# Kernel tuning notes

Measured on AMD Instinct MI355X. Metric: run time of the kernel, lower is better.

## Reference

```python
import jax, jax.numpy as jnp
import numpy as np

B, S, HID = 2, 2048, 2048
NH, NKV = 32, 8
HD = HID // NH          # 64
G = NH // NKV           # 4 query heads per kv head
ROPE_BASE = 10000.0


def _rope_cos_sin(seq_len, head_dim, dtype):
    inv_freq = 1.0 / (ROPE_BASE ** (jnp.arange(0, head_dim, 2, dtype=jnp.float32) / head_dim))
    freqs = jnp.arange(seq_len, dtype=jnp.float32)[:, None] * inv_freq[None, :]  # [S, HD/2]
    cos = jnp.cos(freqs)
    sin = jnp.sin(freqs)
    # torch code does cos.repeat(1, 2): tile along last dim -> [S, HD]
    cos = jnp.concatenate([cos, cos], axis=-1).astype(dtype)
    sin = jnp.concatenate([sin, sin], axis=-1).astype(dtype)
    return cos, sin


def _rotate_half(x):
    x1, x2 = jnp.split(x, 2, axis=-1)
    return jnp.concatenate([-x2, x1], axis=-1)


def setup_inputs() -> dict:
    key = jax.random.key(0)
    ks = jax.random.split(key, 5)
    sc = 0.02
    return {
        "hidden_states": jax.random.normal(ks[0], (B, S, HID), dtype=jnp.float32),
        "wq": jax.random.normal(ks[1], (HID, HID), dtype=jnp.float32) * sc,
        "wk": jax.random.normal(ks[2], (NKV * HD, HID), dtype=jnp.float32) * sc,
        "wv": jax.random.normal(ks[3], (NKV * HD, HID), dtype=jnp.float32) * sc,
        "wo": jax.random.normal(ks[4], (HID, HID), dtype=jnp.float32) * sc,
    }


def reference(hidden_states, wq, wk, wv, wo):
    b, s, _ = hidden_states.shape
    # projections (torch Linear: y = x @ W^T)
    q = (hidden_states @ wq.T).reshape(b, s, NH, HD).transpose(0, 2, 1, 3)   # [B,NH,S,HD]
    k = (hidden_states @ wk.T).reshape(b, s, NKV, HD).transpose(0, 2, 1, 3)  # [B,NKV,S,HD]
    v = (hidden_states @ wv.T).reshape(b, s, NKV, HD).transpose(0, 2, 1, 3)  # [B,NKV,S,HD]

    cos, sin = _rope_cos_sin(s, HD, q.dtype)  # [S,HD]
    q = q * cos + _rotate_half(q) * sin
    k = k * cos + _rotate_half(k) * sin

    # GQA: group query heads per kv head instead of repeat_interleave (same math)
    qg = q.reshape(b, NKV, G, s, HD)
    scale = HD ** -0.5
    scores = jnp.einsum('bkgsd,bktd->bkgst', qg, k) * scale     # [B,NKV,G,S,S]
    attn = jax.nn.softmax(scores, axis=-1)
    out = jnp.einsum('bkgst,bktd->bkgsd', attn, v)              # [B,NKV,G,S,HD]
    out = out.reshape(b, NH, s, HD).transpose(0, 2, 1, 3).reshape(b, s, HID)
    return out @ wo.T
```

## Files before the change

kernel.cpp:

```cpp
#include <hip/hip_runtime.h>
#include <stdint.h>

typedef __attribute__((ext_vector_type(8))) short bf16x8;
typedef __attribute__((ext_vector_type(4))) short bf16x4;
typedef __attribute__((ext_vector_type(4))) float f32x4;
typedef __attribute__((ext_vector_type(4))) unsigned u32x4;
typedef __attribute__((ext_vector_type(2))) unsigned u32x2;

#define S_LEN 2048
#define HIDDEN 2048
#define N_HEADS 32
#define N_KV 8
#define HEAD_DIM 64
#define KVD (N_KV * HEAD_DIM)

__device__ __forceinline__ float bf2f(short u) {
  return __builtin_bit_cast(float, ((unsigned)(unsigned short)u) << 16);
}
__device__ __forceinline__ short f2bf(float f) {
  unsigned u = __builtin_bit_cast(unsigned, f);
  u += 0x7FFFu + ((u >> 16) & 1u);
  return (short)(u >> 16);
}
__device__ __forceinline__ unsigned cvtpk(float lo, float hi) {
  unsigned r;
  asm("v_cvt_pk_bf16_f32 %0, %1, %2" : "=v"(r) : "v"(lo), "v"(hi));
  return r;
}
__device__ __forceinline__ bf16x8 cvt8(f32x4 lo, f32x4 hi) {
  bf16x8 r;
#pragma unroll
  for (int j = 0; j < 4; ++j) { r[j] = f2bf(lo[j]); r[j + 4] = f2bf(hi[j]); }
  return r;
}
__device__ __forceinline__ void storeC(float* p, float v) { *p = v; }
__device__ __forceinline__ void storeC(short* p, float v) { *p = f2bf(v); }

__device__ __forceinline__ void gll16(const void* g, void* l) {
  __builtin_amdgcn_global_load_lds(
      (const __attribute__((address_space(1))) void*)g,
      (__attribute__((address_space(3))) void*)l, 16, 0, 0);
}

struct CvtArgs {
  const float* src[5];
  short* dst[5];
  int cnt4[5];
};
__global__ void cvt_bf16(CvtArgs a, int total4) {
  int u = blockIdx.x * 256 + threadIdx.x;
  const int stride = gridDim.x * 256;
  for (; u < total4; u += stride) {
    int s = 0, off = u;
    while (off >= a.cnt4[s]) { off -= a.cnt4[s]; ++s; }
    f32x4 v = *(const f32x4*)(a.src[s] + (size_t)off * 4);
    bf16x4 r;
#pragma unroll
    for (int j = 0; j < 4; ++j) r[j] = f2bf(v[j]);
    *(bf16x4*)(a.dst[s] + (size_t)off * 4) = r;
  }
}

template <typename CT>
__launch_bounds__(256, 3)
__global__ void gemm_lds(const short* __restrict__ A, const short* __restrict__ W,
                         CT* __restrict__ C, int M, int N, int K) {
  __shared__ short As[128 * 32];
  __shared__ short Ws[128 * 32];
  const int tid  = threadIdx.x;
  const int lane = tid & 63;
  const int w    = tid >> 6;
  const int wm = w >> 1, wn = w & 1;
  const int lr = lane & 15, lg = lane >> 4;
  const int m0 = blockIdx.y * 128, n0 = blockIdx.x * 128;

  const size_t a0 = (size_t)(m0 + w * 16 + (lane >> 2)) * K + (lane & 3) * 8;
  const size_t a1 = a0 + (size_t)64 * K;
  const size_t b0 = (size_t)(n0 + w * 16 + (lane >> 2)) * K + (lane & 3) * 8;
  const size_t b1 = b0 + (size_t)64 * K;
  short* lA0 = &As[(w * 16) * 32];
  short* lA1 = &As[(64 + w * 16) * 32];
  short* lB0 = &Ws[(w * 16) * 32];
  short* lB1 = &Ws[(64 + w * 16) * 32];

  f32x4 acc[4][4] = {};

  for (int k0 = 0; k0 < K; k0 += 32) {
    __syncthreads();
    gll16(A + a0 + k0, lA0);
    gll16(A + a1 + k0, lA1);
    gll16(W + b0 + k0, lB0);
    gll16(W + b1 + k0, lB1);
    __syncthreads();
    bf16x8 af[4], bfr[4];
#pragma unroll
    for (int i = 0; i < 4; ++i) {
      af[i]  = *(const bf16x8*)&As[(wm * 64 + i * 16 + lr) * 32 + lg * 8];
      bfr[i] = *(const bf16x8*)&Ws[(wn * 64 + i * 16 + lr) * 32 + lg * 8];
    }
#pragma unroll
    for (int i = 0; i < 4; ++i)
#pragma unroll
      for (int j = 0; j < 4; ++j)
        acc[i][j] = __builtin_amdgcn_mfma_f32_16x16x32_bf16(af[i], bfr[j], acc[i][j], 0, 0, 0);
  }

#pragma unroll
  for (int i = 0; i < 4; ++i)
#pragma unroll
    for (int j = 0; j < 4; ++j) {
      const int row = m0 + wm * 64 + i * 16 + lg * 4;
      const int col = n0 + wn * 64 + j * 16 + lr;
#pragma unroll
      for (int r = 0; r < 4; ++r)
        storeC(&C[(size_t)(row + r) * N + col], acc[i][j][r]);
    }
}

template <typename AT, typename CT>
__launch_bounds__(256, 2)
__global__ void gemm_bt(const AT* __restrict__ A, const float* __restrict__ W,
                        CT* __restrict__ C, int M, int N, int K) {
  __shared__ short As[128][40];
  __shared__ short Ws[128][40];
  const int tid  = threadIdx.x;
  const int lane = tid & 63;
  const int wid  = tid >> 6;
  const int wm = wid >> 1, wn = wid & 1;
  const int lr = lane & 15, lg = lane >> 4;
  const int m0 = blockIdx.y * 128, n0 = blockIdx.x * 128;
  const int srow = tid >> 2;
  const int scol = (tid & 3) * 8;

  f32x4 acc[4][4] = {};
  const AT*    Ap = A + (size_t)(m0 + srow) * K + scol;
  const float* Wp = W + (size_t)(n0 + srow) * K + scol;

  for (int k0 = 0; k0 < K; k0 += 32) {
    bf16x8 a0, a1, b0, b1;
    if constexpr (sizeof(AT) == 4) {
      a0 = cvt8(*(const f32x4*)(Ap + k0), *(const f32x4*)(Ap + k0 + 4));
      a1 = cvt8(*(const f32x4*)(Ap + (size_t)64 * K + k0),
                *(const f32x4*)(Ap + (size_t)64 * K + k0 + 4));
    } else {
      a0 = *(const bf16x8*)(Ap + k0);
      a1 = *(const bf16x8*)(Ap + (size_t)64 * K + k0);
    }
    b0 = cvt8(*(const f32x4*)(Wp + k0), *(const f32x4*)(Wp + k0 + 4));
    b1 = cvt8(*(const f32x4*)(Wp + (size_t)64 * K + k0),
              *(const f32x4*)(Wp + (size_t)64 * K + k0 + 4));
    __syncthreads();
    *(bf16x8*)&As[srow][scol]      = a0;
    *(bf16x8*)&As[srow + 64][scol] = a1;
    *(bf16x8*)&Ws[srow][scol]      = b0;
    *(bf16x8*)&Ws[srow + 64][scol] = b1;
    __syncthreads();
    bf16x8 af[4], bfr[4];
#pragma unroll
    for (int i = 0; i < 4; ++i) {
      af[i]  = *(const bf16x8*)&As[wm * 64 + i * 16 + lr][lg * 8];
      bfr[i] = *(const bf16x8*)&Ws[wn * 64 + i * 16 + lr][lg * 8];
    }
#pragma unroll
    for (int i = 0; i < 4; ++i)
#pragma unroll
      for (int j = 0; j < 4; ++j)
        acc[i][j] = __builtin_amdgcn_mfma_f32_16x16x32_bf16(af[i], bfr[j], acc[i][j], 0, 0, 0);
  }
#pragma unroll
  for (int i = 0; i < 4; ++i)
#pragma unroll
    for (int j = 0; j < 4; ++j) {
      const int row = m0 + wm * 64 + i * 16 + lg * 4;
      const int col = n0 + wn * 64 + j * 16 + lr;
#pragma unroll
      for (int r = 0; r < 4; ++r)
        storeC(&C[(size_t)(row + r) * N + col], acc[i][j][r]);
    }
}

template <int NH>
__global__ void rope_kernel(short* __restrict__ buf, int rowstride, int total) {
  int idx = blockIdx.x * 256 + threadIdx.x;
  if (idx >= total) return;
  const int i   = idx & 31;
  const int hh  = (idx >> 5) % NH;
  const int row = (idx >> 5) / NH;
  const int pos = row & (S_LEN - 1);
  const float invf = exp2f(-(float)i * (13.287712379549449f / 32.0f));
  const float ang  = (float)pos * invf;
  float sn, c;
  sincosf(ang, &sn, &c);
  size_t base = (size_t)row * rowstride + hh * 64;
  float x1 = bf2f(buf[base + i]);
  float x2 = bf2f(buf[base + i + 32]);
  buf[base + i]      = f2bf(x1 * c - x2 * sn);
  buf[base + i + 32] = f2bf(x2 * c + x1 * sn);
}

__device__ __forceinline__ void qkt_mfma(const bf16x8 (&kf)[4][2],
                                         const bf16x8 (&qa)[2][2],
                                         f32x4 (&sf)[2][4]) {
  __builtin_amdgcn_s_setprio(1);
#pragma unroll
  for (int nf = 0; nf < 4; ++nf)
#pragma unroll
    for (int fr = 0; fr < 2; ++fr) {
      f32x4 t = {};
      t = __builtin_amdgcn_mfma_f32_16x16x32_bf16(kf[nf][0], qa[fr][0], t, 0, 0, 0);
      t = __builtin_amdgcn_mfma_f32_16x16x32_bf16(kf[nf][1], qa[fr][1], t, 0, 0, 0);
      sf[fr][nf] = t;
    }
  __builtin_amdgcn_s_setprio(0);
}

template <int KS>
__device__ __forceinline__ void load_kf(bf16x8 (&kf)[4][2], const short* kbase, int t) {
  const short* kp = kbase + (size_t)t * 64 * KS;
#pragma unroll
  for (int nf = 0; nf < 4; ++nf) {
    kf[nf][0] = *(const bf16x8*)(kp + (size_t)nf * 16 * KS);
    kf[nf][1] = *(const bf16x8*)(kp + (size_t)nf * 16 * KS + 32);
  }
}

__device__ __forceinline__ void load_vb(bf16x8 (&vb)[2][4], const short (*vt)[72],
                                        int lr, int lg) {
#pragma unroll
  for (int ks2 = 0; ks2 < 2; ++ks2)
#pragma unroll
    for (int df = 0; df < 4; ++df)
      vb[ks2][df] = *(const bf16x8*)&vt[df * 16 + lr][ks2 * 32 + lg * 8];
}

__device__ __forceinline__ void softmax_pv(
    f32x4 (&sf)[2][4], const bf16x8 (&vb)[2][4], f32x4 (&o)[2][4],
    float (&mrow)[2], float (&msc)[2], float (&lsum)[2],
    float SC, float THRR) {
  bf16x8 pa[2][2];
#pragma unroll
  for (int fr = 0; fr < 2; ++fr) {
    float lmax = fmaxf(fmaxf(sf[fr][0][0], sf[fr][0][1]), fmaxf(sf[fr][0][2], sf[fr][0][3]));
#pragma unroll
    for (int nf = 1; nf < 4; ++nf) {
      float m01 = fmaxf(sf[fr][nf][0], sf[fr][nf][1]);
      float m23 = fmaxf(sf[fr][nf][2], sf[fr][nf][3]);
      lmax = fmaxf(lmax, fmaxf(m01, m23));
    }
    if (!__all(lmax <= mrow[fr] + THRR)) {
      float mx = fmaxf(lmax, __shfl_xor(lmax, 16));
      mx = fmaxf(mx, __shfl_xor(mx, 32));
      const float mnew  = fmaxf(mrow[fr], mx);
      const float alpha = exp2f((mrow[fr] - mnew) * SC);
      mrow[fr] = mnew;
      msc[fr]  = mnew * SC;
      lsum[fr] *= alpha;
#pragma unroll
      for (int df = 0; df < 4; ++df) o[fr][df] *= alpha;
    }
    const float nm = msc[fr];
    float s = 0.f;
#pragma unroll
    for (int nf = 0; nf < 4; ++nf)
#pragma unroll
      for (int r = 0; r < 4; ++r) {
        float pv = exp2f(fmaf(sf[fr][nf][r], SC, -nm));
        sf[fr][nf][r] = pv;
        s += pv;
      }
    lsum[fr] += s;
#pragma unroll
    for (int ks2 = 0; ks2 < 2; ++ks2) {
      u32x4 pk;
      pk[0] = cvtpk(sf[fr][2 * ks2][0], sf[fr][2 * ks2][1]);
      pk[1] = cvtpk(sf[fr][2 * ks2][2], sf[fr][2 * ks2][3]);
      pk[2] = cvtpk(sf[fr][2 * ks2 + 1][0], sf[fr][2 * ks2 + 1][1]);
      pk[3] = cvtpk(sf[fr][2 * ks2 + 1][2], sf[fr][2 * ks2 + 1][3]);
      pa[fr][ks2] = __builtin_bit_cast(bf16x8, pk);
    }
  }
  __builtin_amdgcn_s_setprio(1);
#pragma unroll
  for (int ks2 = 0; ks2 < 2; ++ks2)
#pragma unroll
    for (int fr = 0; fr < 2; ++fr)
#pragma unroll
      for (int df = 0; df < 4; ++df)
        o[fr][df] = __builtin_amdgcn_mfma_f32_16x16x32_bf16(vb[ks2][df], pa[fr][ks2], o[fr][df], 0, 0, 0);
  __builtin_amdgcn_s_setprio(0);
}

#define NT (S_LEN / 64)
template <int QS, int KS, int OS>
__launch_bounds__(256, 2)
__global__ void attn_kernel(const short* __restrict__ Q, const short* __restrict__ K,
                            const short* __restrict__ V, short* __restrict__ O) {
  const int qt = blockIdx.x, h = blockIdx.y, b = blockIdx.z;
  const int kv = h >> 2;
  const int tid  = threadIdx.x;
  const int lane = tid & 63, w = tid >> 6;
  const int lr = lane & 15, lg = lane >> 4;

  __shared__ short Vt[2][64][72];

  const int q0 = qt * 128 + w * 32;
  bf16x8 qa[2][2];
#pragma unroll
  for (int fr = 0; fr < 2; ++fr) {
    const short* qp = Q + (size_t)(b * S_LEN + q0 + fr * 16 + lr) * QS + h * HEAD_DIM + lg * 8;
    qa[fr][0] = *(const bf16x8*)qp;
    qa[fr][1] = *(const bf16x8*)(qp + 32);
  }

  f32x4 o[2][4] = {};
  float mrow[2] = {-1e30f, -1e30f};
  float msc[2]  = {-1e30f, -1e30f};
  float lsum[2] = {0.f, 0.f};

  const int vdb   = w * 16;
  const int cperm = (lane & 32) + ((lane >> 2) & 3) * 8 + ((lane >> 4) & 1) * 4 + (lane & 3);
  const short* vbase = V + ((size_t)(b * S_LEN) + lane) * KS + kv * HEAD_DIM + vdb;
  const short* kbase = K + (size_t)(b * S_LEN + lr) * KS + kv * HEAD_DIM + lg * 8;

  const float SC   = 0.125f * 1.4426950408889634f;
  const float THRR = 8.0f / SC;

  bf16x8 vp0 = *(const bf16x8*)vbase;
  bf16x8 vp1 = *(const bf16x8*)(vbase + 8);
  bf16x8 kf[4][2];
  bf16x8 vbA[2][4], vbB[2][4];
  f32x4 sfA[2][4], sfB[2][4];
  load_kf<KS>(kf, kbase, 0);
  qkt_mfma(kf, qa, sfA);
  load_kf<KS>(kf, kbase, 1);

  for (int t = 0; t < NT; t += 2) {
#pragma unroll
    for (int j = 0; j < 8; ++j) Vt[0][vdb + j][cperm] = vp0[j];
#pragma unroll
    for (int j = 0; j < 8; ++j) Vt[0][vdb + 8 + j][cperm] = vp1[j];
    __syncthreads();
    load_vb(vbA, Vt[0], lr, lg);
    {
      const short* vp = vbase + (size_t)(t + 1) * 64 * KS;
      vp0 = *(const bf16x8*)vp;
      vp1 = *(const bf16x8*)(vp + 8);
    }
    qkt_mfma(kf, qa, sfB);
    if (t + 2 < NT) load_kf<KS>(kf, kbase, t + 2);
    softmax_pv(sfA, vbA, o, mrow, msc, lsum, SC, THRR);

#pragma unroll
    for (int j = 0; j < 8; ++j) Vt[1][vdb + j][cperm] = vp0[j];
#pragma unroll
    for (int j = 0; j < 8; ++j) Vt[1][vdb + 8 + j][cperm] = vp1[j];
    __syncthreads();
    load_vb(vbB, Vt[1], lr, lg);
    if (t + 2 < NT) {
      const short* vp = vbase + (size_t)(t + 2) * 64 * KS;
      vp0 = *(const bf16x8*)vp;
      vp1 = *(const bf16x8*)(vp + 8);
      qkt_mfma(kf, qa, sfA);
    }
    if (t + 3 < NT) load_kf<KS>(kf, kbase, t + 3);
    softmax_pv(sfB, vbB, o, mrow, msc, lsum, SC, THRR);
  }

#pragma unroll
  for (int fr = 0; fr < 2; ++fr) {
    float ls = lsum[fr];
    ls += __shfl_xor(ls, 16);
    ls += __shfl_xor(ls, 32);
    const float invl = 1.0f / ls;
    const size_t orow = (size_t)(b * S_LEN + q0 + fr * 16 + lr) * OS + h * HEAD_DIM;
#pragma unroll
    for (int df = 0; df < 4; ++df) {
      u32x2 pk;
      pk[0] = cvtpk(o[fr][df][0] * invl, o[fr][df][1] * invl);
      pk[1] = cvtpk(o[fr][df][2] * invl, o[fr][df][3] * invl);
      *(u32x2*)&O[orow + df * 16 + 4 * lg] = pk;
    }
  }
}

extern "C" void kernel_launch(void* const* d_in, const int* in_sizes, int n_in,
                              void* d_out, int out_size, void* d_ws, size_t ws_size,
                              hipStream_t stream) {
  (void)in_sizes; (void)n_in; (void)out_size;
  const float* hidden = (const float*)d_in[0];
  const float* wq = (const float*)d_in[1];
  const float* wk = (const float*)d_in[2];
  const float* wv = (const float*)d_in[3];
  const float* wo = (const float*)d_in[4];
  float* out = (float*)d_out;

  const int M = 2 * S_LEN;
  const size_t nHid  = (size_t)M * HIDDEN;
  const size_t nW    = (size_t)HIDDEN * HIDDEN;
  const size_t nWkv  = (size_t)KVD * HIDDEN;
  const size_t nWcat = nW + 2 * nWkv;
  const int    NQKV  = HIDDEN + 2 * KVD;
  const size_t nQKV  = (size_t)M * NQKV;

  const size_t fastElems = nHid + nWcat + nW + nQKV + nHid;
  if (ws_size >= fastElems * sizeof(short)) {
    short* hb   = (short*)d_ws;
    short* wcat = hb + nHid;
    short* wob  = wcat + nWcat;
    short* QKV  = wob + nW;
    short* AO   = QKV + nQKV;

    CvtArgs ca;
    ca.src[0] = hidden; ca.dst[0] = hb;            ca.cnt4[0] = (int)(nHid / 4);
    ca.src[1] = wq;     ca.dst[1] = wcat;          ca.cnt4[1] = (int)(nW / 4);
    ca.src[2] = wk;     ca.dst[2] = wcat + nW;     ca.cnt4[2] = (int)(nWkv / 4);
    ca.src[3] = wv;     ca.dst[3] = wcat + nW + nWkv; ca.cnt4[3] = (int)(nWkv / 4);
    ca.src[4] = wo;     ca.dst[4] = wob;           ca.cnt4[4] = (int)(nW / 4);
    const int total4 = (int)((nHid + nWcat + nW) / 4);
    cvt_bf16<<<2048, 256, 0, stream>>>(ca, total4);

    gemm_lds<short><<<dim3(NQKV / 128, 32), 256, 0, stream>>>(hb, wcat, QKV, M, NQKV, HIDDEN);
    const int rtot = M * 40 * 32;
    rope_kernel<40><<<(rtot + 255) / 256, 256, 0, stream>>>(QKV, NQKV, rtot);
    attn_kernel<3072, 3072, HIDDEN><<<dim3(S_LEN / 128, N_HEADS, 2), 256, 0, stream>>>(
        QKV, QKV + HIDDEN, QKV + HIDDEN + KVD, AO);
    gemm_lds<float><<<dim3(16, 32), 256, 0, stream>>>(AO, wob, out, M, HIDDEN, HIDDEN);
  } else {
    short* Qb = (short*)d_ws;
    short* Kb = Qb + nHid;
    short* Vb = Kb + (size_t)M * KVD;
    short* AO = Vb + (size_t)M * KVD;
    gemm_bt<float, short><<<dim3(16, 32), 256, 0, stream>>>(hidden, wq, Qb, M, HIDDEN, HIDDEN);
    gemm_bt<float, short><<<dim3(4, 32), 256, 0, stream>>>(hidden, wk, Kb, M, KVD, HIDDEN);
    gemm_bt<float, short><<<dim3(4, 32), 256, 0, stream>>>(hidden, wv, Vb, M, KVD, HIDDEN);
    const int rq = M * N_HEADS * 32, rk = M * N_KV * 32;
    rope_kernel<N_HEADS><<<(rq + 255) / 256, 256, 0, stream>>>(Qb, HIDDEN, rq);
    rope_kernel<N_KV><<<(rk + 255) / 256, 256, 0, stream>>>(Kb, KVD, rk);
    attn_kernel<HIDDEN, KVD, HIDDEN><<<dim3(S_LEN / 128, N_HEADS, 2), 256, 0, stream>>>(
        Qb, Kb, Vb, AO);
    gemm_bt<short, float><<<dim3(16, 32), 256, 0, stream>>>(AO, wo, out, M, HIDDEN, HIDDEN);
  }
}
```

Measured before the change: 289.1 us.

## Pre-transpose V into MFMA-ready global layout and drop in-kernel LDS transpose

Adds a separate vtrans kernel that writes V transposed and permuted per 64-key tile into a scratch buffer reusing the hidden-state bf16 area. The attention kernel then loads V fragments directly from global memory instead of scattering V into shared memory with two __syncthreads per tile pair, which removes the LDS traffic and barriers. In exchange it adds a kernel launch and an extra pass over V. V loads are now uncovered global reads issued right before use, with less prefetch distance. The softmax row sum is also switched to a tree reduction.

```diff
diff --git a/kernel.cpp b/kernel.cpp
--- a/kernel.cpp
+++ b/kernel.cpp
@@ -198,6 +198,34 @@
   buf[base + i + 32] = f2bf(x2 * c + x1 * sn);
 }
 
+__global__ void vtrans(const short* __restrict__ Vsrc, int vs, short* __restrict__ Vtp) {
+  const int t = blockIdx.x, kv = blockIdx.y, b = blockIdx.z;
+  __shared__ short lt[64][72];
+  const int kl = threadIdx.x >> 2;
+  const int dq = (threadIdx.x & 3) * 16;
+  const short* src = Vsrc + (size_t)(b * S_LEN + t * 64 + kl) * vs + kv * 64 + dq;
+  bf16x8 v0 = *(const bf16x8*)src;
+  bf16x8 v1 = *(const bf16x8*)(src + 8);
+  *(bf16x8*)&lt[kl][dq]     = v0;
+  *(bf16x8*)&lt[kl][dq + 8] = v1;
+  __syncthreads();
+  const int d  = threadIdx.x >> 2;
+  const int cb = (threadIdx.x & 3) * 16;
+  bf16x8 o0, o1;
+#pragma unroll
+  for (int j = 0; j < 8; ++j) {
+    const int c  = cb + j;
+    const int k  = (c & 32) | (((c >> 2) & 1) << 4) | (((c >> 3) & 3) << 2) | (c & 3);
+    o0[j] = lt[k][d];
+    const int c2 = cb + 8 + j;
+    const int k2 = (c2 & 32) | (((c2 >> 2) & 1) << 4) | (((c2 >> 3) & 3) << 2) | (c2 & 3);
+    o1[j] = lt[k2][d];
+  }
+  short* dst = Vtp + (size_t)((b * N_KV + kv) * 64 + d) * S_LEN + t * 64 + cb;
+  *(bf16x8*)dst       = o0;
+  *(bf16x8*)(dst + 8) = o1;
+}
+
 __device__ __forceinline__ void qkt_mfma(const bf16x8 (&kf)[4][2],
                                          const bf16x8 (&qa)[2][2],
                                          f32x4 (&sf)[2][4]) {
@@ -224,13 +252,14 @@
   }
 }
 
-__device__ __forceinline__ void load_vb(bf16x8 (&vb)[2][4], const short (*vt)[72],
-                                        int lr, int lg) {
+__device__ __forceinline__ void load_vbg(bf16x8 (&vb)[2][4], const short* vtbase,
+                                         int t, int lr, int lg) {
 #pragma unroll
   for (int ks2 = 0; ks2 < 2; ++ks2)
 #pragma unroll
     for (int df = 0; df < 4; ++df)
-      vb[ks2][df] = *(const bf16x8*)&vt[df * 16 + lr][ks2 * 32 + lg * 8];
+      vb[ks2][df] = *(const bf16x8*)(vtbase + (size_t)(df * 16 + lr) * S_LEN
+                                     + t * 64 + ks2 * 32 + lg * 8);
 }
 
 __device__ __forceinline__ void softmax_pv(
@@ -259,16 +288,18 @@
       for (int df = 0; df < 4; ++df) o[fr][df] *= alpha;
     }
     const float nm = msc[fr];
-    float s = 0.f;
 #pragma unroll
     for (int nf = 0; nf < 4; ++nf)
 #pragma unroll
-      for (int r = 0; r < 4; ++r) {
-        float pv = exp2f(fmaf(sf[fr][nf][r], SC, -nm));
-        sf[fr][nf][r] = pv;
-        s += pv;
-      }
-    lsum[fr] += s;
+      for (int r = 0; r < 4; ++r)
+        sf[fr][nf][r] = exp2f(fmaf(sf[fr][nf][r], SC, -nm));
+    {
+      float t0 = (sf[fr][0][0] + sf[fr][0][1]) + (sf[fr][0][2] + sf[fr][0][3]);
+      float t1 = (sf[fr][1][0] + sf[fr][1][1]) + (sf[fr][1][2] + sf[fr][1][3]);
+      float t2 = (sf[fr][2][0] + sf[fr][2][1]) + (sf[fr][2][2] + sf[fr][2][3]);
+      float t3 = (sf[fr][3][0] + sf[fr][3][1]) + (sf[fr][3][2] + sf[fr][3][3]);
+      lsum[fr] += (t0 + t1) + (t2 + t3);
+    }
 #pragma unroll
     for (int ks2 = 0; ks2 < 2; ++ks2) {
       u32x4 pk;
@@ -294,15 +325,13 @@
 template <int QS, int KS, int OS>
 __launch_bounds__(256, 2)
 __global__ void attn_kernel(const short* __restrict__ Q, const short* __restrict__ K,
-                            const short* __restrict__ V, short* __restrict__ O) {
+                            const short* __restrict__ Vtp, short* __restrict__ O) {
   const int qt = blockIdx.x, h = blockIdx.y, b = blockIdx.z;
   const int kv = h >> 2;
   const int tid  = threadIdx.x;
   const int lane = tid & 63, w = tid >> 6;
   const int lr = lane & 15, lg = lane >> 4;
 
-  __shared__ short Vt[2][64][72];
-
   const int q0 = qt * 128 + w * 32;
   bf16x8 qa[2][2];
 #pragma unroll
@@ -317,53 +346,31 @@
   float msc[2]  = {-1e30f, -1e30f};
   float lsum[2] = {0.f, 0.f};
 
-  const int vdb   = w * 16;
-  const int cperm = (lane & 32) + ((lane >> 2) & 3) * 8 + ((lane >> 4) & 1) * 4 + (lane & 3);
-  const short* vbase = V + ((size_t)(b * S_LEN) + lane) * KS + kv * HEAD_DIM + vdb;
-  const short* kbase = K + (size_t)(b * S_LEN + lr) * KS + kv * HEAD_DIM + lg * 8;
+  const short* vtbase = Vtp + (size_t)((b * N_KV + kv) * 64) * S_LEN;
+  const short* kbase  = K + (size_t)(b * S_LEN + lr) * KS + kv * HEAD_DIM + lg * 8;
 
   const float SC   = 0.125f * 1.4426950408889634f;
   const float THRR = 8.0f / SC;
 
-  bf16x8 vp0 = *(const bf16x8*)vbase;
-  bf16x8 vp1 = *(const bf16x8*)(vbase + 8);
   bf16x8 kf[4][2];
-  bf16x8 vbA[2][4], vbB[2][4];
+  bf16x8 vb[2][4];
   f32x4 sfA[2][4], sfB[2][4];
   load_kf<KS>(kf, kbase, 0);
   qkt_mfma(kf, qa, sfA);
   load_kf<KS>(kf, kbase, 1);
 
   for (int t = 0; t < NT; t += 2) {
-#pragma unroll
-    for (int j = 0; j < 8; ++j) Vt[0][vdb + j][cperm] = vp0[j];
-#pragma unroll
-    for (int j = 0; j < 8; ++j) Vt[0][vdb + 8 + j][cperm] = vp1[j];
-    __syncthreads();
-    load_vb(vbA, Vt[0], lr, lg);
-    {
-      const short* vp = vbase + (size_t)(t + 1) * 64 * KS;
-      vp0 = *(const bf16x8*)vp;
-      vp1 = *(const bf16x8*)(vp + 8);
-    }
+    load_vbg(vb, vtbase, t, lr, lg);
     qkt_mfma(kf, qa, sfB);
     if (t + 2 < NT) load_kf<KS>(kf, kbase, t + 2);
-    softmax_pv(sfA, vbA, o, mrow, msc, lsum, SC, THRR);
-
-#pragma unroll
-    for (int j = 0; j < 8; ++j) Vt[1][vdb + j][cperm] = vp0[j];
-#pragma unroll
-    for (int j = 0; j < 8; ++j) Vt[1][vdb + 8 + j][cperm] = vp1[j];
-    __syncthreads();
-    load_vb(vbB, Vt[1], lr, lg);
+    softmax_pv(sfA, vb, o, mrow, msc, lsum, SC, THRR);
+
+    load_vbg(vb, vtbase, t + 1, lr, lg);
     if (t + 2 < NT) {
-      const short* vp = vbase + (size_t)(t + 2) * 64 * KS;
-      vp0 = *(const bf16x8*)vp;
-      vp1 = *(const bf16x8*)(vp + 8);
       qkt_mfma(kf, qa, sfA);
-    }
-    if (t + 3 < NT) load_kf<KS>(kf, kbase, t + 3);
-    softmax_pv(sfB, vbB, o, mrow, msc, lsum, SC, THRR);
+      if (t + 3 < NT) load_kf<KS>(kf, kbase, t + 3);
+    }
+    softmax_pv(sfB, vb, o, mrow, msc, lsum, SC, THRR);
   }
 
 #pragma unroll
@@ -401,6 +408,7 @@
   const size_t nWcat = nW + 2 * nWkv;
   const int    NQKV  = HIDDEN + 2 * KVD;
   const size_t nQKV  = (size_t)M * NQKV;
+  const size_t nVtp  = (size_t)M * KVD;
 
   const size_t fastElems = nHid + nWcat + nW + nQKV + nHid;
   if (ws_size >= fastElems * sizeof(short)) {
@@ -409,6 +417,7 @@
     short* wob  = wcat + nWcat;
     short* QKV  = wob + nW;
     short* AO   = QKV + nQKV;
+    short* vtp  = hb;
 
     CvtArgs ca;
     ca.src[0] = hidden; ca.dst[0] = hb;            ca.cnt4[0] = (int)(nHid / 4);
@@ -420,24 +429,27 @@
     cvt_bf16<<<2048, 256, 0, stream>>>(ca, total4);
 
     gemm_lds<short><<<dim3(NQKV / 128, 32), 256, 0, stream>>>(hb, wcat, QKV, M, NQKV, HIDDEN);
+    vtrans<<<dim3(S_LEN / 64, N_KV, 2), 256, 0, stream>>>(QKV + HIDDEN + KVD, NQKV, vtp);
     const int rtot = M * 40 * 32;
     rope_kernel<40><<<(rtot + 255) / 256, 256, 0, stream>>>(QKV, NQKV, rtot);
     attn_kernel<3072, 3072, HIDDEN><<<dim3(S_LEN / 128, N_HEADS, 2), 256, 0, stream>>>(
-        QKV, QKV + HIDDEN, QKV + HIDDEN + KVD, AO);
+        QKV, QKV + HIDDEN, vtp, AO);
     gemm_lds<float><<<dim3(16, 32), 256, 0, stream>>>(AO, wob, out, M, HIDDEN, HIDDEN);
   } else {
-    short* Qb = (short*)d_ws;
-    short* Kb = Qb + nHid;
-    short* Vb = Kb + (size_t)M * KVD;
-    short* AO = Vb + (size_t)M * KVD;
+    short* Qb  = (short*)d_ws;
+    short* Kb  = Qb + nHid;
+    short* Vb  = Kb + nVtp;
+    short* AO  = Vb + nVtp;
+    short* vtp = AO + nHid;
     gemm_bt<float, short><<<dim3(16, 32), 256, 0, stream>>>(hidden, wq, Qb, M, HIDDEN, HIDDEN);
     gemm_bt<float, short><<<dim3(4, 32), 256, 0, stream>>>(hidden, wk, Kb, M, KVD, HIDDEN);
     gemm_bt<float, short><<<dim3(4, 32), 256, 0, stream>>>(hidden, wv, Vb, M, KVD, HIDDEN);
     const int rq = M * N_HEADS * 32, rk = M * N_KV * 32;
     rope_kernel<N_HEADS><<<(rq + 255) / 256, 256, 0, stream>>>(Qb, HIDDEN, rq);
     rope_kernel<N_KV><<<(rk + 255) / 256, 256, 0, stream>>>(Kb, KVD, rk);
+    vtrans<<<dim3(S_LEN / 64, N_KV, 2), 256, 0, stream>>>(Vb, KVD, vtp);
     attn_kernel<HIDDEN, KVD, HIDDEN><<<dim3(S_LEN / 128, N_HEADS, 2), 256, 0, stream>>>(
-        Qb, Kb, Vb, AO);
+        Qb, Kb, vtp, AO);
     gemm_bt<short, float><<<dim3(16, 32), 256, 0, stream>>>(AO, wo, out, M, HIDDEN, HIDDEN);
   }
 }
```

Measured after the change: 369.3 us. 1.28x slower.
